# Optimization experiments

Hardware: AMD Instinct MI355X
Metric: run time of the kernel (lower is better)

The kernel has to match this reference:

```python
import jax, jax.numpy as jnp
from jax import lax
import numpy as np

IGNORE_INDEX = -100


def setup_inputs() -> dict:
    key = jax.random.key(0)
    k1, k2, k3 = jax.random.split(key, 3)
    N, D, V = 8192, 2048, 32000
    x = jax.random.normal(k1, (N, D), dtype=jnp.float32) * (D ** -0.5)
    proj_weight = jax.random.normal(k2, (V, D), dtype=jnp.float32) * (D ** -0.5)
    target = jax.random.randint(k3, (N,), 0, V, dtype=jnp.int64 if jax.config.jax_enable_x64 else jnp.int32)
    return {"x": x, "proj_weight": proj_weight, "target": target, "num_splits": 4}


def reference(x, proj_weight, target, num_splits):
    # Fused linear-projection + cross-entropy, chunked over the token dim so the
    # full [N, V] logits tensor is never materialized (only [N/num_splits, V]).
    N, D = x.shape
    chunk = N // num_splits  # N chosen divisible by num_splits
    x_c = x.reshape(num_splits, chunk, D)
    t_c = target.reshape(num_splits, chunk)

    def body(carry, inp):
        loss_sum, count = carry
        xi, ti = inp  # [chunk, D], [chunk]
        logits = jnp.einsum('nd,vd->nv', xi, proj_weight)  # [chunk, V]
        lse = jax.nn.logsumexp(logits, axis=-1)            # [chunk]
        valid = ti != IGNORE_INDEX
        safe_t = jnp.where(valid, ti, 0)
        tgt_logit = jnp.take_along_axis(logits, safe_t[:, None], axis=-1)[:, 0]
        loss = jnp.where(valid, lse - tgt_logit, 0.0)
        return (loss_sum + loss.sum(), count + valid.sum()), None

    init = (jnp.float32(0.0), jnp.int32(0))
    (loss_sum, count), _ = lax.scan(body, init, (x_c, t_c))
    return loss_sum / count.astype(jnp.float32)  # mean over non-ignored tokens
```

## Files before the change

kernel.cpp:

```cpp
#include <hip/hip_runtime.h>
#include <hip/hip_bf16.h>


typedef __bf16 bf16_t;
typedef bf16_t bf16x8 __attribute__((ext_vector_type(8)));
typedef float f32x4 __attribute__((ext_vector_type(4)));

constexpr int N_TOK = 8192;
constexpr int DIM   = 2048;
constexpr int VOCAB = 32000;
constexpr int BM = 256, BN = 256, BK = 64;
constexpr int MT  = N_TOK / BM;
constexpr int NVT = VOCAB / BN;
constexpr int NKT = DIM / BK;
constexpr int IGNORE_INDEX = -100;

#define GPTR(p) ((const __attribute__((address_space(1))) void*)(p))
#define LPTR(p) ((__attribute__((address_space(3))) void*)(p))

__device__ __forceinline__ bf16_t f2bf(float f) {
  union { float f; unsigned u; } in; in.f = f;
  unsigned u = in.u;
  unsigned r = u + 0x7fffu + ((u >> 16) & 1u);
  union { unsigned short s; bf16_t b; } out;
  out.s = (unsigned short)(r >> 16);
  return out.b;
}

constexpr int XN8 = N_TOK * DIM / 8;
constexpr int WN8 = VOCAB * DIM / 8;
constexpr int CVT_BLOCKS = 2048;

__global__ __launch_bounds__(256) void cvt_both(const float* __restrict__ x,
                                                const float* __restrict__ w,
                                                bf16_t* __restrict__ xb,
                                                bf16_t* __restrict__ wb) {
  for (int i = blockIdx.x * 256 + threadIdx.x; i < XN8 + WN8; i += CVT_BLOCKS * 256) {
    const float* src; bf16_t* dst; int j;
    if (i < XN8) { src = x; dst = xb; j = i; }
    else { src = w; dst = wb; j = i - XN8; }
    const float4* s = (const float4*)src;
    float4 a = s[2 * (size_t)j], b = s[2 * (size_t)j + 1];
    bf16x8 o;
    o[0] = f2bf(a.x); o[1] = f2bf(a.y); o[2] = f2bf(a.z); o[3] = f2bf(a.w);
    o[4] = f2bf(b.x); o[5] = f2bf(b.y); o[6] = f2bf(b.z); o[7] = f2bf(b.w);
    *(bf16x8*)(dst + (size_t)j * 8) = o;
  }
}

__device__ __forceinline__ void stage_half(const bf16_t* rowbase, int ktile,
                                           char* smem, int ldsoff, int tid) {
#pragma unroll
  for (int i = 0; i < 2; ++i) {
    int c = i * 512 + tid;
    int row = c >> 3, cin = c & 7;
    int sc = cin ^ (row & 7);
    const bf16_t* g = rowbase + (size_t)row * DIM + ktile * BK + sc * 8;
    __builtin_amdgcn_global_load_lds(GPTR(g), LPTR(smem + ldsoff + c * 16), 16, 0, 0);
  }
}

template <int SLOT>
__device__ __forceinline__ bf16x8 ldA(const char* smem, int row, int ks, int lg) {
  int ch = (ks * 4 + lg) ^ (row & 7);
  return *(const bf16x8*)(smem + SLOT + row * 128 + ch * 16);
}
template <int SLOT>
__device__ __forceinline__ bf16x8 ldB(const char* smem, int row, int ks, int lg) {
  int ch = (ks * 4 + lg) ^ (row & 7);
  return *(const bf16x8*)(smem + SLOT + 32768 + row * 128 + ch * 16);
}

#define MFMA_Q(AVEC, BVEC, MOFF, NOFF)                                          \
  __builtin_amdgcn_s_setprio(1);                                                \
  _Pragma("unroll") for (int ks = 0; ks < 2; ++ks)                              \
    _Pragma("unroll") for (int m = 0; m < 4; ++m)                               \
      _Pragma("unroll") for (int n = 0; n < 2; ++n)                             \
        acc[m + MOFF][n + NOFF] = __builtin_amdgcn_mfma_f32_16x16x32_bf16(      \
            AVEC[m][ks], BVEC[n][ks], acc[m + MOFF][n + NOFF], 0, 0, 0);        \
  __builtin_amdgcn_s_setprio(0);

#define PRE_MFMA()                                    \
  __builtin_amdgcn_s_barrier();                       \
  asm volatile("s_waitcnt lgkmcnt(0)" ::: "memory");

template <int CUR, int NXT>
__device__ __forceinline__ void tile_body(
    int ktB, int ktA, const bf16_t* Abase, const bf16_t* Bbase, char* smem,
    int tid, int wr, int wc, int l15, int lg,
    bf16x8 (&alo)[4][2], bf16x8 (&ahi)[4][2],
    bf16x8 (&b01)[2][2], bf16x8 (&b23)[2][2], f32x4 (&acc)[8][4]) {
#pragma unroll
  for (int m = 0; m < 4; ++m)
#pragma unroll
    for (int ks = 0; ks < 2; ++ks)
      alo[m][ks] = ldA<CUR>(smem, wr * 128 + m * 16 + l15, ks, lg);
#pragma unroll
  for (int n = 0; n < 2; ++n)
#pragma unroll
    for (int ks = 0; ks < 2; ++ks)
      b01[n][ks] = ldB<CUR>(smem, wc * 64 + n * 16 + l15, ks, lg);
  stage_half(Bbase, ktB, smem, NXT + 32768, tid);
  asm volatile("s_waitcnt vmcnt(4)" ::: "memory");
  PRE_MFMA();
  MFMA_Q(alo, b01, 0, 0);
  __builtin_amdgcn_s_barrier();

#pragma unroll
  for (int m = 0; m < 4; ++m)
#pragma unroll
    for (int ks = 0; ks < 2; ++ks)
      ahi[m][ks] = ldA<CUR>(smem, wr * 128 + 64 + m * 16 + l15, ks, lg);
  stage_half(Bbase + 128 * DIM, ktB, smem, NXT + 49152, tid);
  PRE_MFMA();
  MFMA_Q(ahi, b01, 4, 0);
  __builtin_amdgcn_s_barrier();

#pragma unroll
  for (int n = 0; n < 2; ++n)
#pragma unroll
    for (int ks = 0; ks < 2; ++ks)
      b23[n][ks] = ldB<CUR>(smem, wc * 64 + (n + 2) * 16 + l15, ks, lg);
  stage_half(Abase, ktA, smem, CUR, tid);
  asm volatile("s_waitcnt vmcnt(4)" ::: "memory");
  PRE_MFMA();
  MFMA_Q(ahi, b23, 4, 2);
  __builtin_amdgcn_s_barrier();

  stage_half(Abase + 128 * DIM, ktA, smem, CUR + 16384, tid);
  PRE_MFMA();
  MFMA_Q(alo, b23, 0, 2);
  __builtin_amdgcn_s_barrier();
}

__global__ __launch_bounds__(512, 2) void fused_gemm_lse(
    const bf16_t* __restrict__ X, const bf16_t* __restrict__ W,
    const int* __restrict__ target,
    float2* __restrict__ partials, float* __restrict__ tgt_logit) {
  __shared__ __align__(16) char smem[131072];

  const int tid  = threadIdx.x;
  const int lane = tid & 63;
  const int wid  = tid >> 6;
  const int wr   = wid >> 2;
  const int wc   = wid & 3;
  const int l15  = lane & 15;
  const int lg   = lane >> 4;

  int bid  = blockIdx.x;
  int wgid = (bid & 7) * (MT * NVT / 8) + (bid >> 3);
  int mt = wgid & (MT - 1);
  int vt = wgid >> 5;
  const int brow = mt * BM;
  const int bcol = vt * BN;

  const bf16_t* Abase = X + (size_t)brow * DIM;
  const bf16_t* Bbase = W + (size_t)bcol * DIM;

  f32x4 acc[8][4];
#pragma unroll
  for (int m = 0; m < 8; ++m)
#pragma unroll
    for (int n = 0; n < 4; ++n)
      acc[m][n] = (f32x4){0.f, 0.f, 0.f, 0.f};
  bf16x8 alo[4][2], ahi[4][2], b01[2][2], b23[2][2];

  stage_half(Abase,             0, smem, 0,             tid);
  stage_half(Abase + 128 * DIM, 0, smem, 16384,         tid);
  stage_half(Bbase,             0, smem, 32768,         tid);
  stage_half(Bbase + 128 * DIM, 0, smem, 49152,         tid);
  stage_half(Abase,             1, smem, 65536,         tid);
  stage_half(Abase + 128 * DIM, 1, smem, 65536 + 16384, tid);
  asm volatile("s_waitcnt vmcnt(4)" ::: "memory");
  __builtin_amdgcn_s_barrier();

  for (int t = 0; t < NKT; t += 2) {
    tile_body<0, 65536>((t + 1) & (NKT - 1), (t + 2) & (NKT - 1),
                        Abase, Bbase, smem, tid, wr, wc, l15, lg,
                        alo, ahi, b01, b23, acc);
    tile_body<65536, 0>((t + 2) & (NKT - 1), (t + 3) & (NKT - 1),
                        Abase, Bbase, smem, tid, wr, wc, l15, lg,
                        alo, ahi, b01, b23, acc);
  }

  __syncthreads();
  float* smax = (float*)smem;
  float* ssum = (float*)(smem + 4096);
#pragma unroll
  for (int m = 0; m < 8; ++m) {
#pragma unroll
    for (int i = 0; i < 4; ++i) {
      int rloc = wr * 128 + m * 16 + lg * 4 + i;
      int grow = brow + rloc;
      int tgt  = target[grow];
      float v0 = acc[m][0][i], v1 = acc[m][1][i], v2 = acc[m][2][i], v3 = acc[m][3][i];
      int colbase = bcol + wc * 64 + l15;
      if (colbase      == tgt) tgt_logit[grow] = v0;
      if (colbase + 16 == tgt) tgt_logit[grow] = v1;
      if (colbase + 32 == tgt) tgt_logit[grow] = v2;
      if (colbase + 48 == tgt) tgt_logit[grow] = v3;
      float rmax = fmaxf(fmaxf(v0, v1), fmaxf(v2, v3));
#pragma unroll
      for (int s = 1; s < 16; s <<= 1) rmax = fmaxf(rmax, __shfl_xor(rmax, s));
      float rsum = __expf(v0 - rmax) + __expf(v1 - rmax) +
                   __expf(v2 - rmax) + __expf(v3 - rmax);
#pragma unroll
      for (int s = 1; s < 16; s <<= 1) rsum += __shfl_xor(rsum, s);
      if (l15 == 0) { smax[rloc * 4 + wc] = rmax; ssum[rloc * 4 + wc] = rsum; }
    }
  }
  __syncthreads();
  if (tid < BM) {
    float M = smax[tid * 4], S = ssum[tid * 4];
#pragma unroll
    for (int c = 1; c < 4; ++c) {
      float m2 = smax[tid * 4 + c], s2 = ssum[tid * 4 + c];
      float Mn = fmaxf(M, m2);
      S = S * __expf(M - Mn) + s2 * __expf(m2 - Mn);
      M = Mn;
    }
    partials[(size_t)(brow + tid) * NVT + vt] = make_float2(M, S);
  }
}

__global__ __launch_bounds__(256) void finalize_rows(
    const float2* __restrict__ partials, const float* __restrict__ tgt_logit,
    const int* __restrict__ target, float2* __restrict__ blocksum) {
  int tid = threadIdx.x, lane = tid & 63, w = tid >> 6;
  int row = blockIdx.x * 4 + w;
  float M = -1e30f, S = 0.f;
  for (int i = lane; i < NVT; i += 64) {
    float2 p = partials[(size_t)row * NVT + i];
    float Mn = fmaxf(M, p.x);
    S = S * __expf(M - Mn) + p.y * __expf(p.x - Mn);
    M = Mn;
  }
#pragma unroll
  for (int s = 1; s < 64; s <<= 1) {
    float Mo = __shfl_xor(M, s), So = __shfl_xor(S, s);
    float Mn = fmaxf(M, Mo);
    S = S * __expf(M - Mn) + So * __expf(Mo - Mn);
    M = Mn;
  }
  __shared__ float ls[4], cs[4];
  if (lane == 0) {
    int t = target[row];
    bool valid = (t != IGNORE_INDEX);
    float lse = M + __logf(S);
    ls[w] = valid ? (lse - tgt_logit[row]) : 0.f;
    cs[w] = valid ? 1.f : 0.f;
  }
  __syncthreads();
  if (tid == 0)
    blocksum[blockIdx.x] = make_float2(ls[0] + ls[1] + ls[2] + ls[3],
                                       cs[0] + cs[1] + cs[2] + cs[3]);
}

__global__ __launch_bounds__(256) void finalize_out(
    const float2* __restrict__ blocksum, float* __restrict__ out) {
  int tid = threadIdx.x;
  float s = 0.f, c = 0.f;
  for (int i = tid; i < N_TOK / 4; i += 256) {
    float2 b = blocksum[i];
    s += b.x; c += b.y;
  }
#pragma unroll
  for (int k = 1; k < 64; k <<= 1) { s += __shfl_xor(s, k); c += __shfl_xor(c, k); }
  __shared__ float ss[4], cc[4];
  int w = tid >> 6;
  if ((tid & 63) == 0) { ss[w] = s; cc[w] = c; }
  __syncthreads();
  if (tid == 0) out[0] = (ss[0] + ss[1] + ss[2] + ss[3]) / (cc[0] + cc[1] + cc[2] + cc[3]);
}

extern "C" void kernel_launch(void* const* d_in, const int* in_sizes, int n_in,
                              void* d_out, int out_size, void* d_ws, size_t ws_size,
                              hipStream_t stream) {
  const float* x = (const float*)d_in[0];
  const float* w = (const float*)d_in[1];
  const int* target = (const int*)d_in[2];
  float* out = (float*)d_out;

  char* ws = (char*)d_ws;
  size_t off = 0;
  bf16_t* Xbf = (bf16_t*)(ws + off); off += (size_t)N_TOK * DIM * 2;
  bf16_t* Wbf = (bf16_t*)(ws + off); off += (size_t)VOCAB * DIM * 2;
  float2* partials = (float2*)(ws + off); off += (size_t)N_TOK * NVT * 8;
  float*  tgtlog   = (float*)(ws + off);  off += (size_t)N_TOK * 4;
  float2* blocksum = (float2*)(ws + off); off += (size_t)(N_TOK / 4) * 8;
  (void)ws_size; (void)in_sizes; (void)n_in; (void)out_size;

  cvt_both<<<CVT_BLOCKS, 256, 0, stream>>>(x, w, Xbf, Wbf);
  fused_gemm_lse<<<MT * NVT, 512, 0, stream>>>(Xbf, Wbf, target, partials, tgtlog);
  finalize_rows<<<N_TOK / 4, 256, 0, stream>>>(partials, tgtlog, target, blocksum);
  finalize_out<<<1, 256, 0, stream>>>(blocksum, out);
}
```

Measured before the change: 1.485 ms.

## Restructure GEMM k-loop into k-half phases with fewer operand registers

Reorganizes each K-tile into four phases split by k-slice (ks=0 then ks=1) instead of by N-half, so only 4 A and 4 B fragments are live at a time rather than 16+8. Staging addresses are precomputed once per thread (toff), and the staging schedule changes: the second A half of the next tile is loaded earlier into the next slot, and the prologue now waits for all loads. sched_barrier fences are added after waitcnts. The intent is to lower register pressure and address arithmetic and to reshape the load/MFMA overlap, at the risk of introducing LDS hazards or less overlap.

Result: faster. 1.441 ms (-3.0%).

```diff
diff --git a/kernel.cpp b/kernel.cpp
--- a/kernel.cpp
+++ b/kernel.cpp
@@ -17,6 +17,13 @@
 
 #define GPTR(p) ((const __attribute__((address_space(1))) void*)(p))
 #define LPTR(p) ((__attribute__((address_space(3))) void*)(p))
+
+#define VMCNT(N)                                            \
+  asm volatile("s_waitcnt vmcnt(" #N ")" ::: "memory");     \
+  __builtin_amdgcn_sched_barrier(0)
+#define LGKM0()                                             \
+  asm volatile("s_waitcnt lgkmcnt(0)" ::: "memory");        \
+  __builtin_amdgcn_sched_barrier(0)
 
 __device__ __forceinline__ bf16_t f2bf(float f) {
   union { float f; unsigned u; } in; in.f = f;
@@ -48,16 +55,12 @@
   }
 }
 
-__device__ __forceinline__ void stage_half(const bf16_t* rowbase, int ktile,
-                                           char* smem, int ldsoff, int tid) {
-#pragma unroll
-  for (int i = 0; i < 2; ++i) {
-    int c = i * 512 + tid;
-    int row = c >> 3, cin = c & 7;
-    int sc = cin ^ (row & 7);
-    const bf16_t* g = rowbase + (size_t)row * DIM + ktile * BK + sc * 8;
-    __builtin_amdgcn_global_load_lds(GPTR(g), LPTR(smem + ldsoff + c * 16), 16, 0, 0);
-  }
+__device__ __forceinline__ void stage_half(const bf16_t* base, int kt,
+                                           long toff, char* smem, int ldsoff,
+                                           int tid) {
+  const bf16_t* g = base + kt * BK + toff;
+  __builtin_amdgcn_global_load_lds(GPTR(g), LPTR(smem + ldsoff + tid * 16), 16, 0, 0);
+  __builtin_amdgcn_global_load_lds(GPTR(g + 64 * DIM), LPTR(smem + ldsoff + 8192 + tid * 16), 16, 0, 0);
 }
 
 template <int SLOT>
@@ -71,65 +74,58 @@
   return *(const bf16x8*)(smem + SLOT + 32768 + row * 128 + ch * 16);
 }
 
-#define MFMA_Q(AVEC, BVEC, MOFF, NOFF)                                          \
-  __builtin_amdgcn_s_setprio(1);                                                \
-  _Pragma("unroll") for (int ks = 0; ks < 2; ++ks)                              \
-    _Pragma("unroll") for (int m = 0; m < 4; ++m)                               \
-      _Pragma("unroll") for (int n = 0; n < 2; ++n)                             \
-        acc[m + MOFF][n + NOFF] = __builtin_amdgcn_mfma_f32_16x16x32_bf16(      \
-            AVEC[m][ks], BVEC[n][ks], acc[m + MOFF][n + NOFF], 0, 0, 0);        \
-  __builtin_amdgcn_s_setprio(0);
-
 #define PRE_MFMA()                                    \
   __builtin_amdgcn_s_barrier();                       \
-  asm volatile("s_waitcnt lgkmcnt(0)" ::: "memory");
+  LGKM0();
+
+#define MFMA_HALF(MOFF)                                                         \
+  __builtin_amdgcn_s_setprio(1);                                                \
+  _Pragma("unroll") for (int m = 0; m < 4; ++m)                                 \
+    _Pragma("unroll") for (int n = 0; n < 4; ++n)                               \
+      acc[m + MOFF][n] = __builtin_amdgcn_mfma_f32_16x16x32_bf16(               \
+          aq[m], bq[n], acc[m + MOFF][n], 0, 0, 0);                             \
+  __builtin_amdgcn_s_setprio(0);
 
 template <int CUR, int NXT>
 __device__ __forceinline__ void tile_body(
-    int ktB, int ktA, const bf16_t* Abase, const bf16_t* Bbase, char* smem,
-    int tid, int wr, int wc, int l15, int lg,
-    bf16x8 (&alo)[4][2], bf16x8 (&ahi)[4][2],
-    bf16x8 (&b01)[2][2], bf16x8 (&b23)[2][2], f32x4 (&acc)[8][4]) {
-#pragma unroll
-  for (int m = 0; m < 4; ++m)
-#pragma unroll
-    for (int ks = 0; ks < 2; ++ks)
-      alo[m][ks] = ldA<CUR>(smem, wr * 128 + m * 16 + l15, ks, lg);
-#pragma unroll
-  for (int n = 0; n < 2; ++n)
-#pragma unroll
-    for (int ks = 0; ks < 2; ++ks)
-      b01[n][ks] = ldB<CUR>(smem, wc * 64 + n * 16 + l15, ks, lg);
-  stage_half(Bbase, ktB, smem, NXT + 32768, tid);
-  asm volatile("s_waitcnt vmcnt(4)" ::: "memory");
-  PRE_MFMA();
-  MFMA_Q(alo, b01, 0, 0);
-  __builtin_amdgcn_s_barrier();
-
-#pragma unroll
-  for (int m = 0; m < 4; ++m)
-#pragma unroll
-    for (int ks = 0; ks < 2; ++ks)
-      ahi[m][ks] = ldA<CUR>(smem, wr * 128 + 64 + m * 16 + l15, ks, lg);
-  stage_half(Bbase + 128 * DIM, ktB, smem, NXT + 49152, tid);
-  PRE_MFMA();
-  MFMA_Q(ahi, b01, 4, 0);
-  __builtin_amdgcn_s_barrier();
-
-#pragma unroll
-  for (int n = 0; n < 2; ++n)
-#pragma unroll
-    for (int ks = 0; ks < 2; ++ks)
-      b23[n][ks] = ldB<CUR>(smem, wc * 64 + (n + 2) * 16 + l15, ks, lg);
-  stage_half(Abase, ktA, smem, CUR, tid);
-  asm volatile("s_waitcnt vmcnt(4)" ::: "memory");
-  PRE_MFMA();
-  MFMA_Q(ahi, b23, 4, 2);
-  __builtin_amdgcn_s_barrier();
-
-  stage_half(Abase + 128 * DIM, ktA, smem, CUR + 16384, tid);
-  PRE_MFMA();
-  MFMA_Q(alo, b23, 0, 2);
+    const bf16_t* Ab, const bf16_t* Bb, int ktB, int ktA2, long toff,
+    char* smem, int tid, int wr, int wc, int l15, int lg, f32x4 (&acc)[8][4]) {
+  bf16x8 aq[4], bq[4];
+  const int arow = wr * 128 + l15;
+  const int brow = wc * 64 + l15;
+
+#pragma unroll
+  for (int m = 0; m < 4; ++m) aq[m] = ldA<CUR>(smem, arow + m * 16, 0, lg);
+#pragma unroll
+  for (int n = 0; n < 4; ++n) bq[n] = ldB<CUR>(smem, brow + n * 16, 0, lg);
+  stage_half(Bb, ktB, toff, smem, NXT + 32768, tid);
+  VMCNT(4);
+  PRE_MFMA();
+  MFMA_HALF(0);
+  __builtin_amdgcn_s_barrier();
+
+#pragma unroll
+  for (int m = 0; m < 4; ++m) aq[m] = ldA<CUR>(smem, arow + 64 + m * 16, 0, lg);
+  stage_half(Bb + 128 * DIM, ktB, toff, smem, NXT + 49152, tid);
+  PRE_MFMA();
+  MFMA_HALF(4);
+  __builtin_amdgcn_s_barrier();
+
+#pragma unroll
+  for (int m = 0; m < 4; ++m) aq[m] = ldA<CUR>(smem, arow + m * 16, 1, lg);
+#pragma unroll
+  for (int n = 0; n < 4; ++n) bq[n] = ldB<CUR>(smem, brow + n * 16, 1, lg);
+  stage_half(Ab + 128 * DIM, ktB, toff, smem, NXT + 16384, tid);
+  PRE_MFMA();
+  MFMA_HALF(0);
+  __builtin_amdgcn_s_barrier();
+
+#pragma unroll
+  for (int m = 0; m < 4; ++m) aq[m] = ldA<CUR>(smem, arow + 64 + m * 16, 1, lg);
+  stage_half(Ab, ktA2, toff, smem, CUR, tid);
+  VMCNT(4);
+  PRE_MFMA();
+  MFMA_HALF(4);
   __builtin_amdgcn_s_barrier();
 }
 
@@ -157,30 +153,30 @@
   const bf16_t* Abase = X + (size_t)brow * DIM;
   const bf16_t* Bbase = W + (size_t)bcol * DIM;
 
+  const int srow = tid >> 3;
+  const int ssc  = (tid & 7) ^ (srow & 7);
+  const long toff = (long)srow * DIM + ssc * 8;
+
   f32x4 acc[8][4];
 #pragma unroll
   for (int m = 0; m < 8; ++m)
 #pragma unroll
     for (int n = 0; n < 4; ++n)
       acc[m][n] = (f32x4){0.f, 0.f, 0.f, 0.f};
-  bf16x8 alo[4][2], ahi[4][2], b01[2][2], b23[2][2];
-
-  stage_half(Abase,             0, smem, 0,             tid);
-  stage_half(Abase + 128 * DIM, 0, smem, 16384,         tid);
-  stage_half(Bbase,             0, smem, 32768,         tid);
-  stage_half(Bbase + 128 * DIM, 0, smem, 49152,         tid);
-  stage_half(Abase,             1, smem, 65536,         tid);
-  stage_half(Abase + 128 * DIM, 1, smem, 65536 + 16384, tid);
-  asm volatile("s_waitcnt vmcnt(4)" ::: "memory");
+
+  stage_half(Abase,             0, toff, smem, 0,     tid);
+  stage_half(Abase + 128 * DIM, 0, toff, smem, 16384, tid);
+  stage_half(Bbase,             0, toff, smem, 32768, tid);
+  stage_half(Bbase + 128 * DIM, 0, toff, smem, 49152, tid);
+  stage_half(Abase,             1, toff, smem, 65536, tid);
+  VMCNT(0);
   __builtin_amdgcn_s_barrier();
 
   for (int t = 0; t < NKT; t += 2) {
-    tile_body<0, 65536>((t + 1) & (NKT - 1), (t + 2) & (NKT - 1),
-                        Abase, Bbase, smem, tid, wr, wc, l15, lg,
-                        alo, ahi, b01, b23, acc);
-    tile_body<65536, 0>((t + 2) & (NKT - 1), (t + 3) & (NKT - 1),
-                        Abase, Bbase, smem, tid, wr, wc, l15, lg,
-                        alo, ahi, b01, b23, acc);
+    tile_body<0, 65536>(Abase, Bbase, (t + 1) & (NKT - 1), (t + 2) & (NKT - 1),
+                        toff, smem, tid, wr, wc, l15, lg, acc);
+    tile_body<65536, 0>(Abase, Bbase, (t + 2) & (NKT - 1), (t + 3) & (NKT - 1),
+                        toff, smem, tid, wr, wc, l15, lg, acc);
   }
 
   __syncthreads();
```
